# Kernel tuning notes

Measured on AMD Instinct MI355X. Metric: run time of the kernel, lower is better.

Reference implementation:

```python
import jax, jax.numpy as jnp
import numpy as np

# Production-scale dims (see shape_source)
N = 100000      # nodes
E = 1600000     # shortest-path edges
I = 128         # in_channels
O = 128         # out_channels
K = 5           # max_distance
BN_EPS = 1e-5
GIN_EPS = 0.0   # eps=0.0, trainable_eps=False


def setup_inputs() -> dict:
    key = jax.random.key(0)
    ks = jax.random.split(key, 10)
    node_embeddings = jax.random.normal(ks[0], (N, I), dtype=jnp.float32)
    edge_index = jax.random.randint(ks[1], (2, E), 0, N)          # [2, E] row/col
    edge_weights = jax.random.randint(ks[2], (E,), 1, K + 1)      # SP distance in 1..K
    hop_coef = jax.random.normal(ks[3], (K,), dtype=jnp.float32)
    W1 = jax.random.normal(ks[4], (I, O), dtype=jnp.float32) / np.sqrt(I).astype(np.float32)
    b1 = jnp.zeros((O,), jnp.float32)
    gamma1 = jnp.ones((O,), jnp.float32)
    beta1 = jnp.zeros((O,), jnp.float32)
    W2 = jax.random.normal(ks[5], (O, O), dtype=jnp.float32) / np.sqrt(O).astype(np.float32)
    b2 = jnp.zeros((O,), jnp.float32)
    gamma2 = jnp.ones((O,), jnp.float32)
    beta2 = jnp.zeros((O,), jnp.float32)
    return {
        "node_embeddings": node_embeddings,
        "edge_index": edge_index,
        "edge_weights": edge_weights,
        "hop_coef": hop_coef,
        "W1": W1, "b1": b1, "gamma1": gamma1, "beta1": beta1,
        "W2": W2, "b2": b2, "gamma2": gamma2, "beta2": beta2,
    }


def _batch_norm(x, gamma, beta):
    # BatchNorm1d in training mode: batch mean, biased batch variance
    mean = x.mean(axis=0)
    var = x.var(axis=0)
    return gamma * (x - mean) * jax.lax.rsqrt(var + BN_EPS) + beta


def reference(node_embeddings, edge_index, edge_weights, hop_coef,
              W1, b1, gamma1, beta1, W2, b2, gamma2, beta2):
    # Fused form of the per-hop loop: each edge with SP distance d contributes
    # softmax(hop_coef)[d-1] * x[col] to out[row]. Identical math to K separate
    # sparse.mm's weighted by hop_weights and summed.
    hop_w = jax.nn.softmax(hop_coef)                               # [K]
    valid = (edge_weights >= 1) & (edge_weights <= K)
    w_e = jnp.where(valid, hop_w[jnp.clip(edge_weights - 1, 0, K - 1)], 0.0)  # [E]
    row, col = edge_index[0], edge_index[1]
    msgs = w_e[:, None] * node_embeddings[col]                     # [E, I] gather
    agg = jnp.zeros_like(node_embeddings).at[row].add(msgs)        # [N, I] scatter-add
    h = (1.0 + GIN_EPS) * node_embeddings + agg                    # GIN combine
    h = jax.nn.relu(_batch_norm(h @ W1 + b1, gamma1, beta1))
    h = jax.nn.relu(_batch_norm(h @ W2 + b2, gamma2, beta2))
    return h
```

## Files before the change

### kernel.cpp

```cpp
#include <hip/hip_runtime.h>
#include <hip/hip_bf16.h>


#define RCAP 64
#define P2B 256
#define BPB 4

typedef __attribute__((ext_vector_type(8))) short short8;
typedef __attribute__((ext_vector_type(4))) float f32x4;

__device__ inline unsigned short f2bf(float v) {
    unsigned int u = __float_as_uint(v);
    return (unsigned short)((u + 0x7fffu + ((u >> 16) & 1u)) >> 16);
}
__device__ inline float bf2f(unsigned int u) { return __uint_as_float(u << 16); }
__device__ inline float bflo(unsigned int u) { return __uint_as_float(u << 16); }
__device__ inline float bfhi(unsigned int u) { return __uint_as_float(u & 0xFFFF0000u); }

__global__ __launch_bounds__(256) void prep_k(
        const float* __restrict__ hc, float* __restrict__ hwp, float* __restrict__ sums,
        const float* __restrict__ W1, const float* __restrict__ W2,
        unsigned short* __restrict__ w1h, unsigned short* __restrict__ w1l,
        unsigned short* __restrict__ w2h, unsigned short* __restrict__ w2l,
        const float4* __restrict__ x4, uint4* __restrict__ xb, int K, long long n8) {
    int b = blockIdx.x, tid = threadIdx.x;
    if (b == 0) {
        sums[tid] = 0.f; sums[tid + 256] = 0.f;
        if (tid == 0) {
            float tmp[8];
            float m = -1e30f;
            for (int k = 0; k < K; ++k) m = fmaxf(m, hc[k]);
            float s = 0.f;
            for (int k = 0; k < K; ++k) { float e = __expf(hc[k] - m); tmp[k] = e; s += e; }
            float inv = 1.f / s;
            for (int k = 0; k < 8; ++k) hwp[k] = 0.f;
            for (int k = 0; k < K; ++k) hwp[k + 1] = tmp[k] * inv;
        }
        return;
    }
    if (b <= 2) {
        const float* W = (b == 2) ? W2 : W1;
        unsigned short* th = (b == 2) ? w2h : w1h;
        unsigned short* tl = (b == 2) ? w2l : w1l;
        for (int i = tid; i < 16384; i += 256) {
            int k = i >> 7, n = i & 127;
            float v = W[k * 128 + n];
            unsigned short hi = f2bf(v);
            th[n * 128 + k] = hi;
            tl[n * 128 + k] = f2bf(v - bf2f(hi));
        }
        return;
    }
    long long g = (long long)(b - 3) * 256 + tid;
    if (g >= n8) return;
    float4 a = x4[g * 2], c = x4[g * 2 + 1];
    union { unsigned short us[8]; uint4 v; } o;
    o.us[0] = f2bf(a.x); o.us[1] = f2bf(a.y); o.us[2] = f2bf(a.z); o.us[3] = f2bf(a.w);
    o.us[4] = f2bf(c.x); o.us[5] = f2bf(c.y); o.us[6] = f2bf(c.z); o.us[7] = f2bf(c.w);
    xb[g] = o.v;
}

__global__ __launch_bounds__(256) void count_k(const int* __restrict__ rows,
        int* __restrict__ C, int E, int per, int nbukp) {
    __shared__ int hist[128];
    int blk = blockIdx.x, tid = threadIdx.x;
    for (int i = tid; i < nbukp; i += 256) hist[i] = 0;
    __syncthreads();
    int e0 = blk * per, e1 = min(E, e0 + per);
    for (int e = e0 + tid; e < e1; e += 256)
        atomicAdd(&hist[rows[e] >> 10], 1);
    __syncthreads();
    for (int i = tid; i < nbukp; i += 256) C[i * P2B + blk] = hist[i];
}

__global__ __launch_bounds__(256) void scan1_k(int* __restrict__ C,
        int* __restrict__ tot, int nbukp, int nblk) {
    __shared__ int buf[256];
    int b = blockIdx.x, tid = threadIdx.x;
    int v = (tid < nblk) ? C[b * P2B + tid] : 0;
    buf[tid] = v;
    __syncthreads();
#pragma unroll
    for (int off = 1; off < 256; off <<= 1) {
        int t = (tid >= off) ? buf[tid - off] : 0;
        __syncthreads();
        buf[tid] += t;
        __syncthreads();
    }
    if (tid < nblk) C[b * P2B + tid] = buf[tid] - v;
    if (tid == 255) tot[b] = buf[255];
}

__global__ __launch_bounds__(256) void scan2_k(const int* __restrict__ tot,
        int* __restrict__ bstart, int nbukp) {
    __shared__ int buf[256];
    int tid = threadIdx.x;
    int v = (tid < nbukp) ? tot[tid] : 0;
    buf[tid] = v;
    __syncthreads();
#pragma unroll
    for (int off = 1; off < 256; off <<= 1) {
        int t = (tid >= off) ? buf[tid - off] : 0;
        __syncthreads();
        buf[tid] += t;
        __syncthreads();
    }
    if (tid < nbukp) bstart[tid] = buf[tid] - v;
    if (tid == 0) bstart[nbukp] = buf[nbukp - 1];
}

__global__ __launch_bounds__(256) void scatter_k(const int* __restrict__ rows,
        const int* __restrict__ cols, const int* __restrict__ ew,
        const int* __restrict__ O, const int* __restrict__ bstart,
        unsigned* __restrict__ bucketed, int E, int per, int nbukp, int K) {
    __shared__ unsigned curs[128];
    int blk = blockIdx.x, tid = threadIdx.x;
    for (int i = tid; i < nbukp; i += 256)
        curs[i] = (unsigned)(O[i * P2B + blk] + bstart[i]);
    __syncthreads();
    int e0 = blk * per, e1 = min(E, e0 + per);
    for (int e = e0 + tid; e < e1; e += 256) {
        int r = rows[e];
        int c = cols[e];
        int d = ew[e];
        if (d < 1 || d > K) d = 0;
        unsigned idx = atomicAdd(&curs[r >> 10], 1u);
        bucketed[idx] = (unsigned)d | ((unsigned)c << 3) | ((unsigned)(r & 1023) << 20);
    }
}

__global__ __launch_bounds__(256) void slot3_k(const unsigned* __restrict__ bucketed,
        const int* __restrict__ bstart, int* __restrict__ cur,
        unsigned* __restrict__ staging, int nbukp) {
    int bucket = blockIdx.x % nbukp, sub = blockIdx.x / nbukp;
    int s0 = bstart[bucket], s1 = bstart[bucket + 1];
    int cnt = s1 - s0;
    int qlo = s0 + (int)((long long)cnt * sub / BPB);
    int qhi = s0 + (int)((long long)cnt * (sub + 1) / BPB);
    int rbase = bucket << 10;
    for (int e = qlo + threadIdx.x; e < qhi; e += 256) {
        unsigned u = bucketed[e];
        int row = rbase + (int)(u >> 20);
        int s = atomicAdd(&cur[row], 1);
        if (s < RCAP)
            staging[((size_t)row << 6) + s] = u & 0xFFFFFu;
    }
}

__global__ __launch_bounds__(256) void slot_k(const int* __restrict__ rows,
        const int* __restrict__ cols, const int* __restrict__ ew,
        int* __restrict__ cur, unsigned* __restrict__ staging, int E, int K) {
    int e = blockIdx.x * 256 + threadIdx.x;
    if (e >= E) return;
    int r = rows[e];
    int d = ew[e];
    if (d < 1 || d > K) d = 0;
    int s = atomicAdd(&cur[r], 1);
    if (s < RCAP)
        staging[((size_t)r << 6) + s] = (unsigned)d | ((unsigned)cols[e] << 3);
}

__global__ __launch_bounds__(256) void gather_k(
        const unsigned short* __restrict__ xb, const unsigned* __restrict__ staging,
        const int* __restrict__ cur, const float* __restrict__ hwp,
        unsigned short* __restrict__ h, int N) {
    __shared__ float hwl[8];
    int tid = threadIdx.x;
    if (tid < 8) hwl[tid] = hwp[tid];
    __syncthreads();
    int wid = (blockIdx.x * 256 + tid) >> 6;
    if (wid >= N) return;
    int lane = tid & 63;
    int g4 = lane >> 4, li = lane & 15;
    int deg = __builtin_amdgcn_readfirstlane(cur[wid]);
    deg = min(deg, RCAP);
    const unsigned* ep = staging + ((size_t)wid << 6);
    const unsigned short* xrow = xb + li * 8;
    float a0 = 0.f, a1 = 0.f, a2 = 0.f, a3 = 0.f;
    float a4 = 0.f, a5 = 0.f, a6 = 0.f, a7 = 0.f;
    if (g4 == 0) {
        uint4 u = *(const uint4*)(xb + (size_t)wid * 128 + li * 8);
        a0 = bflo(u.x); a1 = bfhi(u.x); a2 = bflo(u.y); a3 = bfhi(u.y);
        a4 = bflo(u.z); a5 = bfhi(u.z); a6 = bflo(u.w); a7 = bfhi(u.w);
    }
    int j = 0;
    for (; j + 16 <= deg; j += 16) {
        unsigned p0 = ep[j + g4];
        unsigned p1 = ep[j + 4 + g4];
        unsigned p2 = ep[j + 8 + g4];
        unsigned p3 = ep[j + 12 + g4];
        uint4 u0 = *(const uint4*)(xrow + (size_t)(p0 >> 3) * 128);
        uint4 u1 = *(const uint4*)(xrow + (size_t)(p1 >> 3) * 128);
        uint4 u2 = *(const uint4*)(xrow + (size_t)(p2 >> 3) * 128);
        uint4 u3 = *(const uint4*)(xrow + (size_t)(p3 >> 3) * 128);
        float w0 = hwl[p0 & 7], w1 = hwl[p1 & 7];
        float w2 = hwl[p2 & 7], w3 = hwl[p3 & 7];
        a0 = fmaf(w0, bflo(u0.x), a0); a1 = fmaf(w0, bfhi(u0.x), a1);
        a2 = fmaf(w0, bflo(u0.y), a2); a3 = fmaf(w0, bfhi(u0.y), a3);
        a4 = fmaf(w0, bflo(u0.z), a4); a5 = fmaf(w0, bfhi(u0.z), a5);
        a6 = fmaf(w0, bflo(u0.w), a6); a7 = fmaf(w0, bfhi(u0.w), a7);
        a0 = fmaf(w1, bflo(u1.x), a0); a1 = fmaf(w1, bfhi(u1.x), a1);
        a2 = fmaf(w1, bflo(u1.y), a2); a3 = fmaf(w1, bfhi(u1.y), a3);
        a4 = fmaf(w1, bflo(u1.z), a4); a5 = fmaf(w1, bfhi(u1.z), a5);
        a6 = fmaf(w1, bflo(u1.w), a6); a7 = fmaf(w1, bfhi(u1.w), a7);
        a0 = fmaf(w2, bflo(u2.x), a0); a1 = fmaf(w2, bfhi(u2.x), a1);
        a2 = fmaf(w2, bflo(u2.y), a2); a3 = fmaf(w2, bfhi(u2.y), a3);
        a4 = fmaf(w2, bflo(u2.z), a4); a5 = fmaf(w2, bfhi(u2.z), a5);
        a6 = fmaf(w2, bflo(u2.w), a6); a7 = fmaf(w2, bfhi(u2.w), a7);
        a0 = fmaf(w3, bflo(u3.x), a0); a1 = fmaf(w3, bfhi(u3.x), a1);
        a2 = fmaf(w3, bflo(u3.y), a2); a3 = fmaf(w3, bfhi(u3.y), a3);
        a4 = fmaf(w3, bflo(u3.z), a4); a5 = fmaf(w3, bfhi(u3.z), a5);
        a6 = fmaf(w3, bflo(u3.w), a6); a7 = fmaf(w3, bfhi(u3.w), a7);
    }
    for (; j + 4 <= deg; j += 4) {
        unsigned p = ep[j + g4];
        uint4 u = *(const uint4*)(xrow + (size_t)(p >> 3) * 128);
        float w = hwl[p & 7];
        a0 = fmaf(w, bflo(u.x), a0); a1 = fmaf(w, bfhi(u.x), a1);
        a2 = fmaf(w, bflo(u.y), a2); a3 = fmaf(w, bfhi(u.y), a3);
        a4 = fmaf(w, bflo(u.z), a4); a5 = fmaf(w, bfhi(u.z), a5);
        a6 = fmaf(w, bflo(u.w), a6); a7 = fmaf(w, bfhi(u.w), a7);
    }
    if (j < deg) {
        int jj = min(j + g4, deg - 1);
        unsigned p = ep[jj];
        float w = (j + g4 < deg) ? hwl[p & 7] : 0.f;
        uint4 u = *(const uint4*)(xrow + (size_t)(p >> 3) * 128);
        a0 = fmaf(w, bflo(u.x), a0); a1 = fmaf(w, bfhi(u.x), a1);
        a2 = fmaf(w, bflo(u.y), a2); a3 = fmaf(w, bfhi(u.y), a3);
        a4 = fmaf(w, bflo(u.z), a4); a5 = fmaf(w, bfhi(u.z), a5);
        a6 = fmaf(w, bflo(u.w), a6); a7 = fmaf(w, bfhi(u.w), a7);
    }
    a0 += __shfl_xor(a0, 16); a1 += __shfl_xor(a1, 16);
    a2 += __shfl_xor(a2, 16); a3 += __shfl_xor(a3, 16);
    a4 += __shfl_xor(a4, 16); a5 += __shfl_xor(a5, 16);
    a6 += __shfl_xor(a6, 16); a7 += __shfl_xor(a7, 16);
    a0 += __shfl_xor(a0, 32); a1 += __shfl_xor(a1, 32);
    a2 += __shfl_xor(a2, 32); a3 += __shfl_xor(a3, 32);
    a4 += __shfl_xor(a4, 32); a5 += __shfl_xor(a5, 32);
    a6 += __shfl_xor(a6, 32); a7 += __shfl_xor(a7, 32);
    if (g4 == 0) {
        uint4 o;
        o.x = (unsigned int)f2bf(a0) | ((unsigned int)f2bf(a1) << 16);
        o.y = (unsigned int)f2bf(a2) | ((unsigned int)f2bf(a3) << 16);
        o.z = (unsigned int)f2bf(a4) | ((unsigned int)f2bf(a5) << 16);
        o.w = (unsigned int)f2bf(a6) | ((unsigned int)f2bf(a7) << 16);
        *(uint4*)(h + (size_t)wid * 128 + li * 8) = o;
    }
}

__global__ __launch_bounds__(256, 4) void gemm_mfma_k(
        const unsigned short* __restrict__ Ain,
        const unsigned short* __restrict__ Bhg, const unsigned short* __restrict__ Blg,
        const float* __restrict__ bias, unsigned short* __restrict__ zout,
        float* __restrict__ sum_out, float* __restrict__ sq_out, int N) {
    __shared__ unsigned short Bs[128 * 136];
    int tid = threadIdx.x;
    int wave = tid >> 6, lane = tid & 63;
    int n16 = lane & 15, q = lane >> 4;
    int rowbase = blockIdx.x * 128 + wave * 32;

    for (int i = tid; i < 2048; i += 256) {
        int n = i >> 4, c = i & 15;
        *(uint4*)&Bs[n * 136 + c * 8] = *(const uint4*)(Bhg + n * 128 + c * 8);
    }

    short8 afr[4][2];
#pragma unroll
    for (int kk = 0; kk < 4; kk++)
#pragma unroll
        for (int mt = 0; mt < 2; mt++) {
            int ar = rowbase + mt * 16 + n16;
            ar = min(ar, N - 1);
            afr[kk][mt] = *(const short8*)(Ain + (size_t)ar * 128 + kk * 32 + q * 8);
        }

    f32x4 acc[2][8];
#pragma unroll
    for (int mt = 0; mt < 2; mt++)
#pragma unroll
        for (int t = 0; t < 8; t++) acc[mt][t] = (f32x4){0.f, 0.f, 0.f, 0.f};

    __syncthreads();
    int ldsb = n16 * 136 + q * 8;
#pragma unroll
    for (int kk = 0; kk < 4; kk++)
#pragma unroll
        for (int t = 0; t < 8; t++) {
            short8 b = *(const short8*)&Bs[t * 16 * 136 + ldsb + kk * 32];
            acc[0][t] = __builtin_amdgcn_mfma_f32_16x16x32_bf16(afr[kk][0], b, acc[0][t], 0, 0, 0);
            acc[1][t] = __builtin_amdgcn_mfma_f32_16x16x32_bf16(afr[kk][1], b, acc[1][t], 0, 0, 0);
        }
    __syncthreads();
    for (int i = tid; i < 2048; i += 256) {
        int n = i >> 4, c = i & 15;
        *(uint4*)&Bs[n * 136 + c * 8] = *(const uint4*)(Blg + n * 128 + c * 8);
    }
    __syncthreads();
#pragma unroll
    for (int kk = 0; kk < 4; kk++)
#pragma unroll
        for (int t = 0; t < 8; t++) {
            short8 b = *(const short8*)&Bs[t * 16 * 136 + ldsb + kk * 32];
            acc[0][t] = __builtin_amdgcn_mfma_f32_16x16x32_bf16(afr[kk][0], b, acc[0][t], 0, 0, 0);
            acc[1][t] = __builtin_amdgcn_mfma_f32_16x16x32_bf16(afr[kk][1], b, acc[1][t], 0, 0, 0);
        }

    float csum[8], csq[8];
#pragma unroll
    for (int t = 0; t < 8; t++) { csum[t] = 0.f; csq[t] = 0.f; }
#pragma unroll
    for (int t = 0; t < 8; t++) {
        int col = n16 + 16 * t;
        float bv = bias[col];
#pragma unroll
        for (int mt = 0; mt < 2; mt++) {
#pragma unroll
            for (int r = 0; r < 4; r++) {
                int row = rowbase + mt * 16 + q * 4 + r;
                if (row < N) {
                    float v = acc[mt][t][r] + bv;
                    zout[(size_t)row * 128 + col] = f2bf(v);
                    csum[t] += v;
                    csq[t] += v * v;
                }
            }
        }
    }
#pragma unroll
    for (int t = 0; t < 8; t++) {
        csum[t] += __shfl_xor(csum[t], 16);
        csum[t] += __shfl_xor(csum[t], 32);
        csq[t] += __shfl_xor(csq[t], 16);
        csq[t] += __shfl_xor(csq[t], 32);
    }
    __syncthreads();
    float* red = (float*)Bs;
    if (q == 0) {
#pragma unroll
        for (int t = 0; t < 8; t++) {
            int col = n16 + 16 * t;
            red[wave * 128 + col] = csum[t];
            red[512 + wave * 128 + col] = csq[t];
        }
    }
    __syncthreads();
    if (tid < 128) {
        float s = 0.f, qq = 0.f;
#pragma unroll
        for (int w = 0; w < 4; w++) {
            s += red[w * 128 + tid];
            qq += red[512 + w * 128 + tid];
        }
        unsafeAtomicAdd(&sum_out[tid], s);
        unsafeAtomicAdd(&sq_out[tid], qq);
    }
}

__global__ __launch_bounds__(256, 4) void gemm_mfma_bn_k(
        const unsigned short* __restrict__ Zin,
        const float* __restrict__ sum_in, const float* __restrict__ sq_in,
        const float* __restrict__ gamma, const float* __restrict__ beta,
        float invN,
        const unsigned short* __restrict__ Bhg, const unsigned short* __restrict__ Blg,
        const float* __restrict__ bias, unsigned short* __restrict__ zout,
        float* __restrict__ sum_out, float* __restrict__ sq_out, int N) {
    __shared__ unsigned short Bs[128 * 136];
    __shared__ float sc[128], sh[128];
    int tid = threadIdx.x;
    int wave = tid >> 6, lane = tid & 63;
    int n16 = lane & 15, q = lane >> 4;
    int rowbase = blockIdx.x * 128 + wave * 32;

    for (int i = tid; i < 2048; i += 256) {
        int n = i >> 4, c = i & 15;
        *(uint4*)&Bs[n * 136 + c * 8] = *(const uint4*)(Bhg + n * 128 + c * 8);
    }
    if (tid < 128) {
        float mean = sum_in[tid] * invN;
        float var = fmaxf(sq_in[tid] * invN - mean * mean, 0.f);
        float s = gamma[tid] * rsqrtf(var + 1e-5f);
        sc[tid] = s;
        sh[tid] = beta[tid] - mean * s;
    }
    __syncthreads();

    short8 afr[4][2];
#pragma unroll
    for (int kk = 0; kk < 4; kk++)
#pragma unroll
        for (int mt = 0; mt < 2; mt++) {
            int ar = rowbase + mt * 16 + n16;
            ar = min(ar, N - 1);
            short8 raw = *(const short8*)(Zin + (size_t)ar * 128 + kk * 32 + q * 8);
            short8 outv;
#pragma unroll
            for (int i = 0; i < 8; i++) {
                int col = kk * 32 + q * 8 + i;
                float f = bf2f((unsigned short)raw[i]);
                float v = fmaxf(fmaf(f, sc[col], sh[col]), 0.f);
                outv[i] = (short)f2bf(v);
            }
            afr[kk][mt] = outv;
        }

    f32x4 acc[2][8];
#pragma unroll
    for (int mt = 0; mt < 2; mt++)
#pragma unroll
        for (int t = 0; t < 8; t++) acc[mt][t] = (f32x4){0.f, 0.f, 0.f, 0.f};

    int ldsb = n16 * 136 + q * 8;
#pragma unroll
    for (int kk = 0; kk < 4; kk++)
#pragma unroll
        for (int t = 0; t < 8; t++) {
            short8 b = *(const short8*)&Bs[t * 16 * 136 + ldsb + kk * 32];
            acc[0][t] = __builtin_amdgcn_mfma_f32_16x16x32_bf16(afr[kk][0], b, acc[0][t], 0, 0, 0);
            acc[1][t] = __builtin_amdgcn_mfma_f32_16x16x32_bf16(afr[kk][1], b, acc[1][t], 0, 0, 0);
        }
    __syncthreads();
    for (int i = tid; i < 2048; i += 256) {
        int n = i >> 4, c = i & 15;
        *(uint4*)&Bs[n * 136 + c * 8] = *(const uint4*)(Blg + n * 128 + c * 8);
    }
    __syncthreads();
#pragma unroll
    for (int kk = 0; kk < 4; kk++)
#pragma unroll
        for (int t = 0; t < 8; t++) {
            short8 b = *(const short8*)&Bs[t * 16 * 136 + ldsb + kk * 32];
            acc[0][t] = __builtin_amdgcn_mfma_f32_16x16x32_bf16(afr[kk][0], b, acc[0][t], 0, 0, 0);
            acc[1][t] = __builtin_amdgcn_mfma_f32_16x16x32_bf16(afr[kk][1], b, acc[1][t], 0, 0, 0);
        }

    float csum[8], csq[8];
#pragma unroll
    for (int t = 0; t < 8; t++) { csum[t] = 0.f; csq[t] = 0.f; }
#pragma unroll
    for (int t = 0; t < 8; t++) {
        int col = n16 + 16 * t;
        float bv = bias[col];
#pragma unroll
        for (int mt = 0; mt < 2; mt++) {
#pragma unroll
            for (int r = 0; r < 4; r++) {
                int row = rowbase + mt * 16 + q * 4 + r;
                if (row < N) {
                    float v = acc[mt][t][r] + bv;
                    zout[(size_t)row * 128 + col] = f2bf(v);
                    csum[t] += v;
                    csq[t] += v * v;
                }
            }
        }
    }
#pragma unroll
    for (int t = 0; t < 8; t++) {
        csum[t] += __shfl_xor(csum[t], 16);
        csum[t] += __shfl_xor(csum[t], 32);
        csq[t] += __shfl_xor(csq[t], 16);
        csq[t] += __shfl_xor(csq[t], 32);
    }
    __syncthreads();
    float* red = (float*)Bs;
    if (q == 0) {
#pragma unroll
        for (int t = 0; t < 8; t++) {
            int col = n16 + 16 * t;
            red[wave * 128 + col] = csum[t];
            red[512 + wave * 128 + col] = csq[t];
        }
    }
    __syncthreads();
    if (tid < 128) {
        float s = 0.f, qq = 0.f;
#pragma unroll
        for (int w = 0; w < 4; w++) {
            s += red[w * 128 + tid];
            qq += red[512 + w * 128 + tid];
        }
        unsafeAtomicAdd(&sum_out[tid], s);
        unsafeAtomicAdd(&sq_out[tid], qq);
    }
}

__global__ __launch_bounds__(256) void bn2_k(const unsigned short* __restrict__ z2,
        const float* __restrict__ sum2, const float* __restrict__ sq2,
        const float* __restrict__ gamma, const float* __restrict__ beta,
        float* __restrict__ out, long long n8, float invN) {
    __shared__ float sc[128], sh[128];
    int tid = threadIdx.x;
    if (tid < 128) {
        float mean = sum2[tid] * invN;
        float var = fmaxf(sq2[tid] * invN - mean * mean, 0.f);
        float s = gamma[tid] * rsqrtf(var + 1e-5f);
        sc[tid] = s;
        sh[tid] = beta[tid] - mean * s;
    }
    __syncthreads();
    long long g = (long long)blockIdx.x * 256 + tid;
    if (g >= n8) return;
    uint4 u = ((const uint4*)z2)[g];
    int cb = (int)((g * 8) & 127);
    float4 s0 = *(const float4*)&sc[cb], s1 = *(const float4*)&sc[cb + 4];
    float4 t0 = *(const float4*)&sh[cb], t1 = *(const float4*)&sh[cb + 4];
    float4 o0, o1;
    o0.x = fmaxf(fmaf(bflo(u.x), s0.x, t0.x), 0.f);
    o0.y = fmaxf(fmaf(bfhi(u.x), s0.y, t0.y), 0.f);
    o0.z = fmaxf(fmaf(bflo(u.y), s0.z, t0.z), 0.f);
    o0.w = fmaxf(fmaf(bfhi(u.y), s0.w, t0.w), 0.f);
    o1.x = fmaxf(fmaf(bflo(u.z), s1.x, t1.x), 0.f);
    o1.y = fmaxf(fmaf(bfhi(u.z), s1.y, t1.y), 0.f);
    o1.z = fmaxf(fmaf(bflo(u.w), s1.z, t1.z), 0.f);
    o1.w = fmaxf(fmaf(bfhi(u.w), s1.w, t1.w), 0.f);
    ((float4*)out)[g * 2] = o0;
    ((float4*)out)[g * 2 + 1] = o1;
}

extern "C" void kernel_launch(void* const* d_in, const int* in_sizes, int n_in,
                              void* d_out, int out_size, void* d_ws, size_t ws_size,
                              hipStream_t stream) {
    const float* x   = (const float*)d_in[0];
    const int*   ei  = (const int*)d_in[1];
    const int*   ew  = (const int*)d_in[2];
    const float* hc  = (const float*)d_in[3];
    const float* W1  = (const float*)d_in[4];
    const float* b1  = (const float*)d_in[5];
    const float* g1  = (const float*)d_in[6];
    const float* be1 = (const float*)d_in[7];
    const float* W2  = (const float*)d_in[8];
    const float* b2  = (const float*)d_in[9];
    const float* g2  = (const float*)d_in[10];
    const float* be2 = (const float*)d_in[11];

    int N = in_sizes[0] / 128;
    int E = in_sizes[2];
    int K = in_sizes[3];
    size_t NF = (size_t)N * 128;
    long long n8 = (long long)(NF / 8);
    int NX = (int)((n8 + 255) / 256);

    unsigned short* h = (unsigned short*)d_ws;
    unsigned short* xb = h + NF;
    unsigned short* z1 = xb;
    unsigned short* z2 = h;
    unsigned* staging = (unsigned*)(xb + NF);
    int* cur = (int*)(staging + (size_t)N * RCAP);
    unsigned short* w1h = (unsigned short*)(cur + N);
    unsigned short* w1l = w1h + 16384;
    unsigned short* w2h = w1l + 16384;
    unsigned short* w2l = w2h + 16384;
    float* hwp = (float*)(w2l + 16384);
    float* sums = hwp + 8;
    float* sum1 = sums, *sq1 = sums + 128, *sum2 = sums + 256, *sq2 = sums + 384;
    int nbuk  = (N + 1023) >> 10;
    int nbukp = (nbuk + 7) & ~7;
    int* C = (int*)(sums + 512);
    int* bstart = C + (size_t)nbukp * P2B;
    int* tot = bstart + nbukp + 1;
    unsigned* bucketed = (unsigned*)(tot + nbukp);
    size_t ws_need = (size_t)((char*)(bucketed + E) - (char*)d_ws);
    bool use_bucketed = (nbukp <= 128) && (N <= (1 << 17)) && (K <= 7)
                        && (ws_need <= ws_size);

    float invN = 1.0f / (float)N;

    hipMemsetAsync(cur, 0, (size_t)N * sizeof(int), stream);

    prep_k<<<3 + NX, 256, 0, stream>>>(hc, hwp, sums, W1, W2,
        w1h, w1l, w2h, w2l, (const float4*)x, (uint4*)xb, K, n8);
    if (use_bucketed) {
        int per = (E + P2B - 1) / P2B;
        count_k<<<P2B, 256, 0, stream>>>(ei, C, E, per, nbukp);
        scan1_k<<<nbukp, 256, 0, stream>>>(C, tot, nbukp, P2B);
        scan2_k<<<1, 256, 0, stream>>>(tot, bstart, nbukp);
        scatter_k<<<P2B, 256, 0, stream>>>(ei, ei + E, ew, C, bstart, bucketed,
                                           E, per, nbukp, K);
        slot3_k<<<nbukp * BPB, 256, 0, stream>>>(bucketed, bstart, cur, staging, nbukp);
    } else {
        slot_k<<<(E + 255) / 256, 256, 0, stream>>>(ei, ei + E, ew, cur, staging, E, K);
    }
    {
        long long tot_thr = (long long)N * 64;
        gather_k<<<(int)((tot_thr + 255) / 256), 256, 0, stream>>>(
            xb, staging, cur, hwp, h, N);
    }
    int gblocks = (N + 127) / 128;
    gemm_mfma_k<<<gblocks, 256, 0, stream>>>(h, w1h, w1l, b1, z1, sum1, sq1, N);
    gemm_mfma_bn_k<<<gblocks, 256, 0, stream>>>(z1, sum1, sq1, g1, be1, invN,
        w2h, w2l, b2, z2, sum2, sq2, N);
    bn2_k<<<NX, 256, 0, stream>>>(z2, sum2, sq2, g2, be2, (float*)d_out, n8, invN);
}
```

Before: 434.3 us.

## Fuse MLP stages into cooperative kernel and merge preprocessing launches

Replaces the two GEMM+BN kernels and the final BN kernel with one cooperative kernel. It keeps accumulators in registers across grid-wide syncs for the batch-norm statistics, so the z1/z2 intermediates never round-trip through global memory. It also folds the count kernel and the cur memset into prep_k, and drops scan2 by recomputing the bucket prefix scan inside scatter and slot3. The cooperative launch needs all 782 blocks to be co-resident and pays for two grid barriers, with a fallback to the old path if the launch fails.

Result: slower. 561.5 us (+29.3%).

```diff
diff --git a/kernel.cpp b/kernel.cpp
--- a/kernel.cpp
+++ b/kernel.cpp
@@ -1,5 +1,6 @@
 #include <hip/hip_runtime.h>
 #include <hip/hip_bf16.h>
+#include <hip/hip_cooperative_groups.h>
 
 
 #define RCAP 64
@@ -22,7 +23,10 @@
         const float* __restrict__ W1, const float* __restrict__ W2,
         unsigned short* __restrict__ w1h, unsigned short* __restrict__ w1l,
         unsigned short* __restrict__ w2h, unsigned short* __restrict__ w2l,
-        const float4* __restrict__ x4, uint4* __restrict__ xb, int K, long long n8) {
+        const float4* __restrict__ x4, uint4* __restrict__ xb, int K, long long n8,
+        const int* __restrict__ rows, int* __restrict__ C, int* __restrict__ cur,
+        int E, int per, int nbukp, int N, int NX) {
+    __shared__ int hist[128];
     int b = blockIdx.x, tid = threadIdx.x;
     if (b == 0) {
         sums[tid] = 0.f; sums[tid + 256] = 0.f;
@@ -51,26 +55,27 @@
         }
         return;
     }
-    long long g = (long long)(b - 3) * 256 + tid;
-    if (g >= n8) return;
-    float4 a = x4[g * 2], c = x4[g * 2 + 1];
-    union { unsigned short us[8]; uint4 v; } o;
-    o.us[0] = f2bf(a.x); o.us[1] = f2bf(a.y); o.us[2] = f2bf(a.z); o.us[3] = f2bf(a.w);
-    o.us[4] = f2bf(c.x); o.us[5] = f2bf(c.y); o.us[6] = f2bf(c.z); o.us[7] = f2bf(c.w);
-    xb[g] = o.v;
-}
-
-__global__ __launch_bounds__(256) void count_k(const int* __restrict__ rows,
-        int* __restrict__ C, int E, int per, int nbukp) {
-    __shared__ int hist[128];
-    int blk = blockIdx.x, tid = threadIdx.x;
+    if (b < 3 + NX) {
+        long long g = (long long)(b - 3) * 256 + tid;
+        if (g >= n8) return;
+        float4 a = x4[g * 2], c = x4[g * 2 + 1];
+        union { unsigned short us[8]; uint4 v; } o;
+        o.us[0] = f2bf(a.x); o.us[1] = f2bf(a.y); o.us[2] = f2bf(a.z); o.us[3] = f2bf(a.w);
+        o.us[4] = f2bf(c.x); o.us[5] = f2bf(c.y); o.us[6] = f2bf(c.z); o.us[7] = f2bf(c.w);
+        xb[g] = o.v;
+        return;
+    }
+    int cblk = b - 3 - NX;
     for (int i = tid; i < nbukp; i += 256) hist[i] = 0;
     __syncthreads();
-    int e0 = blk * per, e1 = min(E, e0 + per);
+    int e0 = cblk * per, e1 = min(E, e0 + per);
     for (int e = e0 + tid; e < e1; e += 256)
         atomicAdd(&hist[rows[e] >> 10], 1);
     __syncthreads();
-    for (int i = tid; i < nbukp; i += 256) C[i * P2B + blk] = hist[i];
+    for (int i = tid; i < nbukp; i += 256) C[i * P2B + cblk] = hist[i];
+    int zper = (N + P2B - 1) / P2B;
+    int z0 = cblk * zper, z1 = min(N, z0 + zper);
+    for (int i = z0 + tid; i < z1; i += 256) cur[i] = 0;
 }
 
 __global__ __launch_bounds__(256) void scan1_k(int* __restrict__ C,
@@ -91,32 +96,25 @@
     if (tid == 255) tot[b] = buf[255];
 }
 
-__global__ __launch_bounds__(256) void scan2_k(const int* __restrict__ tot,
-        int* __restrict__ bstart, int nbukp) {
-    __shared__ int buf[256];
-    int tid = threadIdx.x;
-    int v = (tid < nbukp) ? tot[tid] : 0;
-    buf[tid] = v;
-    __syncthreads();
-#pragma unroll
-    for (int off = 1; off < 256; off <<= 1) {
-        int t = (tid >= off) ? buf[tid - off] : 0;
-        __syncthreads();
-        buf[tid] += t;
-        __syncthreads();
-    }
-    if (tid < nbukp) bstart[tid] = buf[tid] - v;
-    if (tid == 0) bstart[nbukp] = buf[nbukp - 1];
-}
-
 __global__ __launch_bounds__(256) void scatter_k(const int* __restrict__ rows,
         const int* __restrict__ cols, const int* __restrict__ ew,
-        const int* __restrict__ O, const int* __restrict__ bstart,
+        const int* __restrict__ O, const int* __restrict__ tot,
         unsigned* __restrict__ bucketed, int E, int per, int nbukp, int K) {
+    __shared__ int buf[128];
     __shared__ unsigned curs[128];
     int blk = blockIdx.x, tid = threadIdx.x;
-    for (int i = tid; i < nbukp; i += 256)
-        curs[i] = (unsigned)(O[i * P2B + blk] + bstart[i]);
+    int v = (tid < 128 && tid < nbukp) ? tot[tid] : 0;
+    if (tid < 128) buf[tid] = v;
+    __syncthreads();
+#pragma unroll
+    for (int off = 1; off < 128; off <<= 1) {
+        int t = (tid >= off && tid < 128) ? buf[tid - off] : 0;
+        __syncthreads();
+        if (tid < 128) buf[tid] += t;
+        __syncthreads();
+    }
+    if (tid < nbukp)
+        curs[tid] = (unsigned)(O[tid * P2B + blk] + buf[tid] - v);
     __syncthreads();
     int e0 = blk * per, e1 = min(E, e0 + per);
     for (int e = e0 + tid; e < e1; e += 256) {
@@ -130,15 +128,27 @@
 }
 
 __global__ __launch_bounds__(256) void slot3_k(const unsigned* __restrict__ bucketed,
-        const int* __restrict__ bstart, int* __restrict__ cur,
+        const int* __restrict__ tot, int* __restrict__ cur,
         unsigned* __restrict__ staging, int nbukp) {
+    __shared__ int buf[128];
+    int tid = threadIdx.x;
+    if (tid < 128) buf[tid] = (tid < nbukp) ? tot[tid] : 0;
+    __syncthreads();
+#pragma unroll
+    for (int off = 1; off < 128; off <<= 1) {
+        int t = (tid >= off && tid < 128) ? buf[tid - off] : 0;
+        __syncthreads();
+        if (tid < 128) buf[tid] += t;
+        __syncthreads();
+    }
     int bucket = blockIdx.x % nbukp, sub = blockIdx.x / nbukp;
-    int s0 = bstart[bucket], s1 = bstart[bucket + 1];
+    int s1 = buf[bucket];
+    int s0 = s1 - tot[bucket];
     int cnt = s1 - s0;
     int qlo = s0 + (int)((long long)cnt * sub / BPB);
     int qhi = s0 + (int)((long long)cnt * (sub + 1) / BPB);
     int rbase = bucket << 10;
-    for (int e = qlo + threadIdx.x; e < qhi; e += 256) {
+    for (int e = qlo + tid; e < qhi; e += 256) {
         unsigned u = bucketed[e];
         int row = rbase + (int)(u >> 20);
         int s = atomicAdd(&cur[row], 1);
@@ -249,6 +259,252 @@
     }
 }
 
+__global__ __launch_bounds__(256, 4) void mlp_coop_k(
+        const unsigned short* __restrict__ Ain,
+        const unsigned short* __restrict__ B1h, const unsigned short* __restrict__ B1l,
+        const float* __restrict__ bias1, const float* __restrict__ gamma1,
+        const float* __restrict__ beta1,
+        const unsigned short* __restrict__ B2h, const unsigned short* __restrict__ B2l,
+        const float* __restrict__ bias2, const float* __restrict__ gamma2,
+        const float* __restrict__ beta2,
+        float* __restrict__ sums, float* __restrict__ outp, float invN, int N) {
+    __shared__ unsigned short Bs[128 * 136];
+    __shared__ float sc[128], sh[128];
+    float* sum1 = sums;       float* sq1 = sums + 128;
+    float* sum2 = sums + 256; float* sq2 = sums + 384;
+    int tid = threadIdx.x;
+    int wave = tid >> 6, lane = tid & 63;
+    int n16 = lane & 15, q = lane >> 4;
+    int rowbase = blockIdx.x * 128 + wave * 32;
+    int ldsb = n16 * 136 + q * 8;
+
+    for (int i = tid; i < 2048; i += 256) {
+        int n = i >> 4, c = i & 15;
+        *(uint4*)&Bs[n * 136 + c * 8] = *(const uint4*)(B1h + n * 128 + c * 8);
+    }
+    short8 afr[4][2];
+#pragma unroll
+    for (int kk = 0; kk < 4; kk++)
+#pragma unroll
+        for (int mt = 0; mt < 2; mt++) {
+            int ar = rowbase + mt * 16 + n16;
+            ar = min(ar, N - 1);
+            afr[kk][mt] = *(const short8*)(Ain + (size_t)ar * 128 + kk * 32 + q * 8);
+        }
+    f32x4 acc[2][8];
+#pragma unroll
+    for (int mt = 0; mt < 2; mt++)
+#pragma unroll
+        for (int t = 0; t < 8; t++) acc[mt][t] = (f32x4){0.f, 0.f, 0.f, 0.f};
+    __syncthreads();
+#pragma unroll
+    for (int kk = 0; kk < 4; kk++)
+#pragma unroll
+        for (int t = 0; t < 8; t++) {
+            short8 b = *(const short8*)&Bs[t * 16 * 136 + ldsb + kk * 32];
+            acc[0][t] = __builtin_amdgcn_mfma_f32_16x16x32_bf16(afr[kk][0], b, acc[0][t], 0, 0, 0);
+            acc[1][t] = __builtin_amdgcn_mfma_f32_16x16x32_bf16(afr[kk][1], b, acc[1][t], 0, 0, 0);
+        }
+    __syncthreads();
+    for (int i = tid; i < 2048; i += 256) {
+        int n = i >> 4, c = i & 15;
+        *(uint4*)&Bs[n * 136 + c * 8] = *(const uint4*)(B1l + n * 128 + c * 8);
+    }
+    __syncthreads();
+#pragma unroll
+    for (int kk = 0; kk < 4; kk++)
+#pragma unroll
+        for (int t = 0; t < 8; t++) {
+            short8 b = *(const short8*)&Bs[t * 16 * 136 + ldsb + kk * 32];
+            acc[0][t] = __builtin_amdgcn_mfma_f32_16x16x32_bf16(afr[kk][0], b, acc[0][t], 0, 0, 0);
+            acc[1][t] = __builtin_amdgcn_mfma_f32_16x16x32_bf16(afr[kk][1], b, acc[1][t], 0, 0, 0);
+        }
+    {
+        float csum[8], csq[8];
+#pragma unroll
+        for (int t = 0; t < 8; t++) { csum[t] = 0.f; csq[t] = 0.f; }
+#pragma unroll
+        for (int t = 0; t < 8; t++) {
+            int col = n16 + 16 * t;
+            float bv = bias1[col];
+#pragma unroll
+            for (int mt = 0; mt < 2; mt++)
+#pragma unroll
+                for (int r = 0; r < 4; r++) {
+                    float v = acc[mt][t][r] + bv;
+                    acc[mt][t][r] = v;
+                    int row = rowbase + mt * 16 + q * 4 + r;
+                    if (row < N) { csum[t] += v; csq[t] += v * v; }
+                }
+        }
+#pragma unroll
+        for (int t = 0; t < 8; t++) {
+            csum[t] += __shfl_xor(csum[t], 16);
+            csum[t] += __shfl_xor(csum[t], 32);
+            csq[t] += __shfl_xor(csq[t], 16);
+            csq[t] += __shfl_xor(csq[t], 32);
+        }
+        __syncthreads();
+        float* red = (float*)Bs;
+        if (q == 0) {
+#pragma unroll
+            for (int t = 0; t < 8; t++) {
+                int col = n16 + 16 * t;
+                red[wave * 128 + col] = csum[t];
+                red[512 + wave * 128 + col] = csq[t];
+            }
+        }
+        __syncthreads();
+        if (tid < 128) {
+            float s = 0.f, qq = 0.f;
+#pragma unroll
+            for (int w = 0; w < 4; w++) {
+                s += red[w * 128 + tid];
+                qq += red[512 + w * 128 + tid];
+            }
+            atomicAdd(&sum1[tid], s);
+            atomicAdd(&sq1[tid], qq);
+        }
+    }
+    cooperative_groups::this_grid().sync();
+
+    if (tid < 128) {
+        float s_ = atomicAdd(&sum1[tid], 0.f);
+        float qq_ = atomicAdd(&sq1[tid], 0.f);
+        float mean = s_ * invN;
+        float var = fmaxf(qq_ * invN - mean * mean, 0.f);
+        float s = gamma1[tid] * rsqrtf(var + 1e-5f);
+        sc[tid] = s;
+        sh[tid] = beta1[tid] - mean * s;
+    }
+    __syncthreads();
+#pragma unroll
+    for (int t = 0; t < 8; t++) {
+        int col = n16 + 16 * t;
+#pragma unroll
+        for (int mt = 0; mt < 2; mt++)
+#pragma unroll
+            for (int r = 0; r < 4; r++) {
+                int lr = wave * 32 + mt * 16 + q * 4 + r;
+                float bn = fmaxf(fmaf(acc[mt][t][r], sc[col], sh[col]), 0.f);
+                Bs[lr * 136 + col] = f2bf(bn);
+            }
+    }
+    __syncthreads();
+#pragma unroll
+    for (int kk = 0; kk < 4; kk++)
+#pragma unroll
+        for (int mt = 0; mt < 2; mt++) {
+            int lr = wave * 32 + mt * 16 + n16;
+            afr[kk][mt] = *(const short8*)&Bs[lr * 136 + kk * 32 + q * 8];
+        }
+    __syncthreads();
+
+    for (int i = tid; i < 2048; i += 256) {
+        int n = i >> 4, c = i & 15;
+        *(uint4*)&Bs[n * 136 + c * 8] = *(const uint4*)(B2h + n * 128 + c * 8);
+    }
+#pragma unroll
+    for (int mt = 0; mt < 2; mt++)
+#pragma unroll
+        for (int t = 0; t < 8; t++) acc[mt][t] = (f32x4){0.f, 0.f, 0.f, 0.f};
+    __syncthreads();
+#pragma unroll
+    for (int kk = 0; kk < 4; kk++)
+#pragma unroll
+        for (int t = 0; t < 8; t++) {
+            short8 b = *(const short8*)&Bs[t * 16 * 136 + ldsb + kk * 32];
+            acc[0][t] = __builtin_amdgcn_mfma_f32_16x16x32_bf16(afr[kk][0], b, acc[0][t], 0, 0, 0);
+            acc[1][t] = __builtin_amdgcn_mfma_f32_16x16x32_bf16(afr[kk][1], b, acc[1][t], 0, 0, 0);
+        }
+    __syncthreads();
+    for (int i = tid; i < 2048; i += 256) {
+        int n = i >> 4, c = i & 15;
+        *(uint4*)&Bs[n * 136 + c * 8] = *(const uint4*)(B2l + n * 128 + c * 8);
+    }
+    __syncthreads();
+#pragma unroll
+    for (int kk = 0; kk < 4; kk++)
+#pragma unroll
+        for (int t = 0; t < 8; t++) {
+            short8 b = *(const short8*)&Bs[t * 16 * 136 + ldsb + kk * 32];
+            acc[0][t] = __builtin_amdgcn_mfma_f32_16x16x32_bf16(afr[kk][0], b, acc[0][t], 0, 0, 0);
+            acc[1][t] = __builtin_amdgcn_mfma_f32_16x16x32_bf16(afr[kk][1], b, acc[1][t], 0, 0, 0);
+        }
+    {
+        float csum[8], csq[8];
+#pragma unroll
+        for (int t = 0; t < 8; t++) { csum[t] = 0.f; csq[t] = 0.f; }
+#pragma unroll
+        for (int t = 0; t < 8; t++) {
+            int col = n16 + 16 * t;
+            float bv = bias2[col];
+#pragma unroll
+            for (int mt = 0; mt < 2; mt++)
+#pragma unroll
+                for (int r = 0; r < 4; r++) {
+                    float v = acc[mt][t][r] + bv;
+                    acc[mt][t][r] = v;
+                    int row = rowbase + mt * 16 + q * 4 + r;
+                    if (row < N) { csum[t] += v; csq[t] += v * v; }
+                }
+        }
+#pragma unroll
+        for (int t = 0; t < 8; t++) {
+            csum[t] += __shfl_xor(csum[t], 16);
+            csum[t] += __shfl_xor(csum[t], 32);
+            csq[t] += __shfl_xor(csq[t], 16);
+            csq[t] += __shfl_xor(csq[t], 32);
+        }
+        __syncthreads();
+        float* red = (float*)Bs;
+        if (q == 0) {
+#pragma unroll
+            for (int t = 0; t < 8; t++) {
+                int col = n16 + 16 * t;
+                red[wave * 128 + col] = csum[t];
+                red[512 + wave * 128 + col] = csq[t];
+            }
+        }
+        __syncthreads();
+        if (tid < 128) {
+            float s = 0.f, qq = 0.f;
+#pragma unroll
+            for (int w = 0; w < 4; w++) {
+                s += red[w * 128 + tid];
+                qq += red[512 + w * 128 + tid];
+            }
+            atomicAdd(&sum2[tid], s);
+            atomicAdd(&sq2[tid], qq);
+        }
+    }
+    cooperative_groups::this_grid().sync();
+
+    if (tid < 128) {
+        float s_ = atomicAdd(&sum2[tid], 0.f);
+        float qq_ = atomicAdd(&sq2[tid], 0.f);
+        float mean = s_ * invN;
+        float var = fmaxf(qq_ * invN - mean * mean, 0.f);
+        float s = gamma2[tid] * rsqrtf(var + 1e-5f);
+        sc[tid] = s;
+        sh[tid] = beta2[tid] - mean * s;
+    }
+    __syncthreads();
+#pragma unroll
+    for (int t = 0; t < 8; t++) {
+        int col = n16 + 16 * t;
+#pragma unroll
+        for (int mt = 0; mt < 2; mt++)
+#pragma unroll
+            for (int r = 0; r < 4; r++) {
+                int row = rowbase + mt * 16 + q * 4 + r;
+                if (row < N)
+                    outp[(size_t)row * 128 + col] =
+                        fmaxf(fmaf(acc[mt][t][r], sc[col], sh[col]), 0.f);
+            }
+    }
+}
+
 __global__ __launch_bounds__(256, 4) void gemm_mfma_k(
         const unsigned short* __restrict__ Ain,
         const unsigned short* __restrict__ Bhg, const unsigned short* __restrict__ Blg,
@@ -259,12 +515,10 @@
     int wave = tid >> 6, lane = tid & 63;
     int n16 = lane & 15, q = lane >> 4;
     int rowbase = blockIdx.x * 128 + wave * 32;
-
     for (int i = tid; i < 2048; i += 256) {
         int n = i >> 4, c = i & 15;
         *(uint4*)&Bs[n * 136 + c * 8] = *(const uint4*)(Bhg + n * 128 + c * 8);
     }
-
     short8 afr[4][2];
 #pragma unroll
     for (int kk = 0; kk < 4; kk++)
@@ -274,13 +528,11 @@
             ar = min(ar, N - 1);
             afr[kk][mt] = *(const short8*)(Ain + (size_t)ar * 128 + kk * 32 + q * 8);
         }
-
     f32x4 acc[2][8];
 #pragma unroll
     for (int mt = 0; mt < 2; mt++)
 #pragma unroll
         for (int t = 0; t < 8; t++) acc[mt][t] = (f32x4){0.f, 0.f, 0.f, 0.f};
-
     __syncthreads();
     int ldsb = n16 * 136 + q * 8;
 #pragma unroll
@@ -305,7 +557,6 @@
             acc[0][t] = __builtin_amdgcn_mfma_f32_16x16x32_bf16(afr[kk][0], b, acc[0][t], 0, 0, 0);
             acc[1][t] = __builtin_amdgcn_mfma_f32_16x16x32_bf16(afr[kk][1], b, acc[1][t], 0, 0, 0);
         }
-
     float csum[8], csq[8];
 #pragma unroll
     for (int t = 0; t < 8; t++) { csum[t] = 0.f; csq[t] = 0.f; }
@@ -371,7 +622,6 @@
     int wave = tid >> 6, lane = tid & 63;
     int n16 = lane & 15, q = lane >> 4;
     int rowbase = blockIdx.x * 128 + wave * 32;
-
     for (int i = tid; i < 2048; i += 256) {
         int n = i >> 4, c = i & 15;
         *(uint4*)&Bs[n * 136 + c * 8] = *(const uint4*)(Bhg + n * 128 + c * 8);
@@ -384,7 +634,6 @@
         sh[tid] = beta[tid] - mean * s;
     }
     __syncthreads();
-
     short8 afr[4][2];
 #pragma unroll
     for (int kk = 0; kk < 4; kk++)
@@ -403,13 +652,11 @@
             }
             afr[kk][mt] = outv;
         }
-
     f32x4 acc[2][8];
 #pragma unroll
     for (int mt = 0; mt < 2; mt++)
 #pragma unroll
         for (int t = 0; t < 8; t++) acc[mt][t] = (f32x4){0.f, 0.f, 0.f, 0.f};
-
     int ldsb = n16 * 136 + q * 8;
 #pragma unroll
     for (int kk = 0; kk < 4; kk++)
@@ -433,7 +680,6 @@
             acc[0][t] = __builtin_amdgcn_mfma_f32_16x16x32_bf16(afr[kk][0], b, acc[0][t], 0, 0, 0);
             acc[1][t] = __builtin_amdgcn_mfma_f32_16x16x32_bf16(afr[kk][1], b, acc[1][t], 0, 0, 0);
         }
-
     float csum[8], csq[8];
 #pragma unroll
     for (int t = 0; t < 8; t++) { csum[t] = 0.f; csq[t] = 0.f; }
@@ -557,27 +803,26 @@
     int nbuk  = (N + 1023) >> 10;
     int nbukp = (nbuk + 7) & ~7;
     int* C = (int*)(sums + 512);
-    int* bstart = C + (size_t)nbukp * P2B;
-    int* tot = bstart + nbukp + 1;
+    int* tot = C + (size_t)nbukp * P2B;
     unsigned* bucketed = (unsigned*)(tot + nbukp);
     size_t ws_need = (size_t)((char*)(bucketed + E) - (char*)d_ws);
     bool use_bucketed = (nbukp <= 128) && (N <= (1 << 17)) && (K <= 7)
                         && (ws_need <= ws_size);
 
     float invN = 1.0f / (float)N;
-
-    hipMemsetAsync(cur, 0, (size_t)N * sizeof(int), stream);
-
-    prep_k<<<3 + NX, 256, 0, stream>>>(hc, hwp, sums, W1, W2,
-        w1h, w1l, w2h, w2l, (const float4*)x, (uint4*)xb, K, n8);
+    int per = (E + P2B - 1) / P2B;
+
+    int prep_grid = use_bucketed ? (3 + NX + P2B) : (3 + NX);
+    if (!use_bucketed)
+        hipMemsetAsync(cur, 0, (size_t)N * sizeof(int), stream);
+    prep_k<<<prep_grid, 256, 0, stream>>>(hc, hwp, sums, W1, W2,
+        w1h, w1l, w2h, w2l, (const float4*)x, (uint4*)xb, K, n8,
+        ei, C, cur, E, per, nbukp, N, NX);
     if (use_bucketed) {
-        int per = (E + P2B - 1) / P2B;
-        count_k<<<P2B, 256, 0, stream>>>(ei, C, E, per, nbukp);
         scan1_k<<<nbukp, 256, 0, stream>>>(C, tot, nbukp, P2B);
-        scan2_k<<<1, 256, 0, stream>>>(tot, bstart, nbukp);
-        scatter_k<<<P2B, 256, 0, stream>>>(ei, ei + E, ew, C, bstart, bucketed,
+        scatter_k<<<P2B, 256, 0, stream>>>(ei, ei + E, ew, C, tot, bucketed,
                                            E, per, nbukp, K);
-        slot3_k<<<nbukp * BPB, 256, 0, stream>>>(bucketed, bstart, cur, staging, nbukp);
+        slot3_k<<<nbukp * BPB, 256, 0, stream>>>(bucketed, tot, cur, staging, nbukp);
     } else {
         slot_k<<<(E + 255) / 256, 256, 0, stream>>>(ei, ei + E, ew, cur, staging, E, K);
     }
@@ -587,8 +832,21 @@
             xb, staging, cur, hwp, h, N);
     }
     int gblocks = (N + 127) / 128;
-    gemm_mfma_k<<<gblocks, 256, 0, stream>>>(h, w1h, w1l, b1, z1, sum1, sq1, N);
-    gemm_mfma_bn_k<<<gblocks, 256, 0, stream>>>(z1, sum1, sq1, g1, be1, invN,
-        w2h, w2l, b2, z2, sum2, sq2, N);
-    bn2_k<<<NX, 256, 0, stream>>>(z2, sum2, sq2, g2, be2, (float*)d_out, n8, invN);
-}
+    float* outf = (float*)d_out;
+    hipError_t ce = hipErrorUnknown;
+    if (gblocks <= 1024) {
+        void* args[] = { (void*)&h, (void*)&w1h, (void*)&w1l,
+                         (void*)&b1, (void*)&g1, (void*)&be1,
+                         (void*)&w2h, (void*)&w2l,
+                         (void*)&b2, (void*)&g2, (void*)&be2,
+                         (void*)&sums, (void*)&outf, (void*)&invN, (void*)&N };
+        ce = hipLaunchCooperativeKernel((const void*)mlp_coop_k,
+                 dim3(gblocks), dim3(256), args, 0, stream);
+    }
+    if (ce != hipSuccess) {
+        gemm_mfma_k<<<gblocks, 256, 0, stream>>>(h, w1h, w1l, b1, z1, sum1, sq1, N);
+        gemm_mfma_bn_k<<<gblocks, 256, 0, stream>>>(z1, sum1, sq1, g1, be1, invN,
+            w2h, w2l, b2, z2, sum2, sq2, N);
+        bn2_k<<<NX, 256, 0, stream>>>(z2, sum2, sq2, g2, be2, outf, n8, invN);
+    }
+}
```
